# Kernel tuning notes

Measured on AMD Instinct MI355X. Metric: run time of the kernel, lower is better.

The kernel has to match this reference:

```python
import jax, jax.numpy as jnp
import numpy as np

B, N, M = 262144, 8, 4  # batch, state dim, measurement dim


def _psd(key, b, d, scale):
    # SPD matrix: A @ A^T / d + 0.1*I  (keeps inverse well-conditioned)
    A = jax.random.normal(key, (b, d, d), dtype=jnp.float32) * scale
    return A @ A.swapaxes(-1, -2) / d + 0.1 * jnp.eye(d, dtype=jnp.float32)


def setup_inputs() -> dict:
    key = jax.random.key(0)
    kF, kH, kS, kQ, kR = jax.random.split(key, 5)
    F = jax.random.normal(kF, (B, N, N), dtype=jnp.float32) * 0.3 + jnp.eye(N, dtype=jnp.float32)
    H = jax.random.normal(kH, (B, M, N), dtype=jnp.float32) * 0.5
    Sigma_previous = _psd(kS, B, N, 1.0)
    Q = _psd(kQ, B, N, 0.3)
    R = _psd(kR, B, M, 0.3)
    return {"F": F, "H": H, "Sigma_previous": Sigma_previous, "Q": Q, "R": R}


def reference(F, H, Sigma_previous, Q, R):
    T = lambda x: x.swapaxes(-1, -2)
    # predicted state covariance: Sigma = F Sigma_prev F^T + Q        [B,N,N]
    Sigma = F @ Sigma_previous @ T(F) + Q
    # innovation covariance: S = H Sigma H^T + R                      [B,M,M]
    S = H @ Sigma @ T(H) + R
    # Kalman gain: KG = Sigma H^T S^{-1}                              [B,N,M]
    P12 = Sigma @ T(H)
    KG = P12 @ jnp.linalg.inv(S)
    return KG
```

## Files before the change

kernel.cpp:

```cpp
#include <hip/hip_runtime.h>


#define NBB 16
#define THREADS 64

__device__ __forceinline__ void gl_lds16(const float* src, float4* dst) {
    __builtin_amdgcn_global_load_lds(
        (const __attribute__((address_space(1))) unsigned int*)src,
        (__attribute__((address_space(3))) unsigned int*)dst,
        16, 0, 0);
}

__global__ __launch_bounds__(THREADS) void kalman_gain_kernel(
    const float* __restrict__ Fg, const float* __restrict__ Hg,
    const float* __restrict__ Spg, const float* __restrict__ Qg,
    const float* __restrict__ Rg, float* __restrict__ out, int nb)
{
    __shared__ float4 smem4[640];

    const int lane = threadIdx.x;
    const int b0   = blockIdx.x * NBB;

    #pragma unroll
    for (int r = 0; r < 4; ++r) {
        int s = (r << 6) | lane;
        int b = s >> 4, j = s & 15, k = j ^ (b & 15);
        gl_lds16(Fg + (size_t)(b0 + b) * 64 + k * 4, smem4 + (r << 6));
    }
    #pragma unroll
    for (int r = 0; r < 2; ++r) {
        int s = (r << 6) | lane;
        int b = s >> 3, j = s & 7, k = j ^ (b & 7);
        gl_lds16(Hg + (size_t)(b0 + b) * 32 + k * 4, smem4 + 512 + (r << 6));
    }
    #pragma unroll
    for (int r = 0; r < 4; ++r) {
        int s = (r << 6) | lane;
        int b = s >> 4, j = s & 15, k = j ^ (b & 15);
        gl_lds16(Spg + (size_t)(b0 + b) * 64 + k * 4, smem4 + 256 + (r << 6));
    }

    const int b_loc = lane >> 2;
    const int p     = lane & 3;
    const int bm15  = b_loc & 15;
    const int bm7   = b_loc & 7;

    const float4 Rr = *(reinterpret_cast<const float4*>(Rg)
                        + (size_t)(b0 + b_loc) * 4 + p);

    __syncthreads();

    float hs[8];
    #pragma unroll
    for (int j = 0; j < 4; ++j) {
        float4 v = smem4[512 + b_loc * 8 + ((2 * j + (p >> 1)) ^ bm7)];
        hs[j*2+0] = (p & 1) ? v.z : v.x;
        hs[j*2+1] = (p & 1) ? v.w : v.y;
    }

    float fr[16];
    #pragma unroll
    for (int i = 0; i < 4; ++i) {
        float4 v = smem4[b_loc * 16 + ((4 * p + i) ^ bm15)];
        fr[i*4+0] = v.x; fr[i*4+1] = v.y; fr[i*4+2] = v.z; fr[i*4+3] = v.w;
    }

    float u[32];
    #pragma unroll
    for (int x = 0; x < 32; ++x) u[x] = 0.f;
    #pragma unroll
    for (int rl = 0; rl < 2; ++rl)
        #pragma unroll
        for (int k = 0; k < 8; ++k)
            #pragma unroll
            for (int j = 0; j < 4; ++j)
                u[k*4+j] += hs[j*2+rl] * fr[rl*8+k];
    #pragma unroll
    for (int x = 0; x < 32; ++x) u[x] += __shfl_xor(u[x], 1, 64);
    #pragma unroll
    for (int x = 0; x < 32; ++x) u[x] += __shfl_xor(u[x], 2, 64);

    __syncthreads();

    #pragma unroll
    for (int r = 0; r < 4; ++r) {
        int s = (r << 6) | lane;
        int b = s >> 4, j = s & 15, k = j ^ (b & 15);
        gl_lds16(Qg + (size_t)(b0 + b) * 64 + k * 4, smem4 + (r << 6));
    }

    float G[16];
    #pragma unroll
    for (int x = 0; x < 16; ++x) G[x] = 0.f;
    #pragma unroll
    for (int k = 0; k < 8; ++k) {
        float4 s0 = smem4[256 + b_loc * 16 + ((2*k    ) ^ bm15)];
        float4 s1 = smem4[256 + b_loc * 16 + ((2*k + 1) ^ bm15)];
        float sp[8] = {s0.x,s0.y,s0.z,s0.w, s1.x,s1.y,s1.z,s1.w};
        #pragma unroll
        for (int il = 0; il < 2; ++il)
            #pragma unroll
            for (int c = 0; c < 8; ++c)
                G[il*8+c] += fr[il*8+k] * sp[c];
    }

    float A[8];
    #pragma unroll
    for (int il = 0; il < 2; ++il)
        #pragma unroll
        for (int j = 0; j < 4; ++j) {
            float acc = 0.f;
            #pragma unroll
            for (int k = 0; k < 8; ++k)
                acc += G[il*8+k] * u[k*4+j];
            A[il*4+j] = acc;
        }

    __syncthreads();

    float qo[16];
    #pragma unroll
    for (int i = 0; i < 4; ++i) {
        float4 v = smem4[b_loc * 16 + ((4 * p + i) ^ bm15)];
        qo[i*4+0] = v.x; qo[i*4+1] = v.y; qo[i*4+2] = v.z; qo[i*4+3] = v.w;
    }
    #pragma unroll
    for (int j = 0; j < 4; ++j) {
        float4 h0 = smem4[512 + b_loc * 8 + ((2*j    ) ^ bm7)];
        float4 h1 = smem4[512 + b_loc * 8 + ((2*j + 1) ^ bm7)];
        float hrow[8] = {h0.x,h0.y,h0.z,h0.w, h1.x,h1.y,h1.z,h1.w};
        #pragma unroll
        for (int il = 0; il < 2; ++il) {
            float acc = 0.f;
            #pragma unroll
            for (int k = 0; k < 8; ++k)
                acc += qo[il*8+k] * hrow[k];
            A[il*4+j] += acc;
        }
    }

    float s[16];
    #pragma unroll
    for (int pi = 0; pi < 4; ++pi) {
        float rrow[4] = {Rr.x, Rr.y, Rr.z, Rr.w};
        #pragma unroll
        for (int q = 0; q < 4; ++q) {
            float acc = (pi == p) ? rrow[q] : 0.f;
            #pragma unroll
            for (int il = 0; il < 2; ++il)
                acc += hs[pi*2+il] * A[il*4+q];
            s[pi*4+q] = acc;
        }
    }
    #pragma unroll
    for (int x = 0; x < 16; ++x) s[x] += __shfl_xor(s[x], 1, 64);
    #pragma unroll
    for (int x = 0; x < 16; ++x) s[x] += __shfl_xor(s[x], 2, 64);

    float is[16] = {1.f,0.f,0.f,0.f, 0.f,1.f,0.f,0.f, 0.f,0.f,1.f,0.f, 0.f,0.f,0.f,1.f};
    #pragma unroll
    for (int c = 0; c < 4; ++c) {
        float pinv = 1.0f / s[c*4+c];
        #pragma unroll
        for (int k = 0; k < 4; ++k) { s[c*4+k] *= pinv; is[c*4+k] *= pinv; }
        #pragma unroll
        for (int r = 0; r < 4; ++r) {
            if (r != c) {
                float fac = s[r*4+c];
                #pragma unroll
                for (int k = 0; k < 4; ++k) {
                    s[r*4+k]  -= fac * s[c*4+k];
                    is[r*4+k] -= fac * is[c*4+k];
                }
            }
        }
    }

    float4* outg = reinterpret_cast<float4*>(out)
                 + (size_t)(b0 + b_loc) * 8 + 2 * p;
    #pragma unroll
    for (int il = 0; il < 2; ++il) {
        float4 o;
        o.x = A[il*4+0]*is[0] + A[il*4+1]*is[4] + A[il*4+2]*is[8]  + A[il*4+3]*is[12];
        o.y = A[il*4+0]*is[1] + A[il*4+1]*is[5] + A[il*4+2]*is[9]  + A[il*4+3]*is[13];
        o.z = A[il*4+0]*is[2] + A[il*4+1]*is[6] + A[il*4+2]*is[10] + A[il*4+3]*is[14];
        o.w = A[il*4+0]*is[3] + A[il*4+1]*is[7] + A[il*4+2]*is[11] + A[il*4+3]*is[15];
        outg[il] = o;
    }
}

extern "C" void kernel_launch(void* const* d_in, const int* in_sizes, int n_in,
                              void* d_out, int out_size, void* d_ws, size_t ws_size,
                              hipStream_t stream) {
    const float* F  = (const float*)d_in[0];
    const float* H  = (const float*)d_in[1];
    const float* Sp = (const float*)d_in[2];
    const float* Q  = (const float*)d_in[3];
    const float* R  = (const float*)d_in[4];
    float* out = (float*)d_out;

    int nb = in_sizes[0] / 64;
    int blocks = nb / NBB;
    kalman_gain_kernel<<<blocks, THREADS, 0, stream>>>(F, H, Sp, Q, R, out, nb);
}
```

Measured before the change: 52.17 us.

## Process multiple tiles per block with double-buffered async LDS prefetch

Each block now loops over 8 tiles of 16 batch elements and uses a double-buffered LDS area. The next tile's F, H, Sigma_prev and R loads are issued while the current tile computes, and manual vmcnt waits replace __syncthreads. R is now staged through LDS as well. The aim is to hide global load latency and cut block launch overhead. In exchange the grid is 8x smaller, which may reduce occupancy and parallelism, and the hand-counted waitcnt values make correctness fragile.

```diff
diff --git a/kernel.cpp b/kernel.cpp
--- a/kernel.cpp
+++ b/kernel.cpp
@@ -3,6 +3,10 @@
 
 #define NBB 16
 #define THREADS 64
+#define TILES 8
+#define BUFG 704
+
+#define WAITV(N) asm volatile("s_waitcnt vmcnt(" #N ")" ::: "memory")
 
 __device__ __forceinline__ void gl_lds16(const float* src, float4* dst) {
     __builtin_amdgcn_global_load_lds(
@@ -11,181 +15,204 @@
         16, 0, 0);
 }
 
+__device__ __forceinline__ void stage_FH(const float* Fg, const float* Hg,
+                                         float4* buf, int gb0, int lane) {
+    #pragma unroll
+    for (int r = 0; r < 4; ++r) {
+        int s = (r << 6) | lane;
+        int b = s >> 4, j = s & 15, k = j ^ (b & 15);
+        gl_lds16(Fg + (size_t)(gb0 + b) * 64 + k * 4, buf + (r << 6));
+    }
+    #pragma unroll
+    for (int r = 0; r < 2; ++r) {
+        int s = (r << 6) | lane;
+        int b = s >> 3, j = s & 7, k = j ^ (b & 7);
+        gl_lds16(Hg + (size_t)(gb0 + b) * 32 + k * 4, buf + 512 + (r << 6));
+    }
+}
+__device__ __forceinline__ void stage_SpR(const float* Spg, const float* Rg,
+                                          float4* buf, int gb0, int lane) {
+    #pragma unroll
+    for (int r = 0; r < 4; ++r) {
+        int s = (r << 6) | lane;
+        int b = s >> 4, j = s & 15, k = j ^ (b & 15);
+        gl_lds16(Spg + (size_t)(gb0 + b) * 64 + k * 4, buf + 256 + (r << 6));
+    }
+    {
+        int s = lane;
+        int b = s >> 2, j = s & 3, k = j ^ (b & 3);
+        gl_lds16(Rg + (size_t)(gb0 + b) * 16 + k * 4, buf + 640);
+    }
+}
+
 __global__ __launch_bounds__(THREADS) void kalman_gain_kernel(
     const float* __restrict__ Fg, const float* __restrict__ Hg,
     const float* __restrict__ Spg, const float* __restrict__ Qg,
     const float* __restrict__ Rg, float* __restrict__ out, int nb)
 {
-    __shared__ float4 smem4[640];
-
-    const int lane = threadIdx.x;
-    const int b0   = blockIdx.x * NBB;
-
-    #pragma unroll
-    for (int r = 0; r < 4; ++r) {
-        int s = (r << 6) | lane;
-        int b = s >> 4, j = s & 15, k = j ^ (b & 15);
-        gl_lds16(Fg + (size_t)(b0 + b) * 64 + k * 4, smem4 + (r << 6));
-    }
-    #pragma unroll
-    for (int r = 0; r < 2; ++r) {
-        int s = (r << 6) | lane;
-        int b = s >> 3, j = s & 7, k = j ^ (b & 7);
-        gl_lds16(Hg + (size_t)(b0 + b) * 32 + k * 4, smem4 + 512 + (r << 6));
-    }
-    #pragma unroll
-    for (int r = 0; r < 4; ++r) {
-        int s = (r << 6) | lane;
-        int b = s >> 4, j = s & 15, k = j ^ (b & 15);
-        gl_lds16(Spg + (size_t)(b0 + b) * 64 + k * 4, smem4 + 256 + (r << 6));
-    }
-
+    __shared__ float4 smem4[2 * BUFG];
+
+    const int lane  = threadIdx.x;
     const int b_loc = lane >> 2;
     const int p     = lane & 3;
     const int bm15  = b_loc & 15;
     const int bm7   = b_loc & 7;
-
-    const float4 Rr = *(reinterpret_cast<const float4*>(Rg)
-                        + (size_t)(b0 + b_loc) * 4 + p);
-
-    __syncthreads();
-
-    float hs[8];
-    #pragma unroll
-    for (int j = 0; j < 4; ++j) {
-        float4 v = smem4[512 + b_loc * 8 + ((2 * j + (p >> 1)) ^ bm7)];
-        hs[j*2+0] = (p & 1) ? v.z : v.x;
-        hs[j*2+1] = (p & 1) ? v.w : v.y;
-    }
-
-    float fr[16];
-    #pragma unroll
-    for (int i = 0; i < 4; ++i) {
-        float4 v = smem4[b_loc * 16 + ((4 * p + i) ^ bm15)];
-        fr[i*4+0] = v.x; fr[i*4+1] = v.y; fr[i*4+2] = v.z; fr[i*4+3] = v.w;
-    }
-
-    float u[32];
-    #pragma unroll
-    for (int x = 0; x < 32; ++x) u[x] = 0.f;
-    #pragma unroll
-    for (int rl = 0; rl < 2; ++rl)
-        #pragma unroll
-        for (int k = 0; k < 8; ++k)
-            #pragma unroll
-            for (int j = 0; j < 4; ++j)
-                u[k*4+j] += hs[j*2+rl] * fr[rl*8+k];
-    #pragma unroll
-    for (int x = 0; x < 32; ++x) u[x] += __shfl_xor(u[x], 1, 64);
-    #pragma unroll
-    for (int x = 0; x < 32; ++x) u[x] += __shfl_xor(u[x], 2, 64);
-
-    __syncthreads();
-
-    #pragma unroll
-    for (int r = 0; r < 4; ++r) {
-        int s = (r << 6) | lane;
-        int b = s >> 4, j = s & 15, k = j ^ (b & 15);
-        gl_lds16(Qg + (size_t)(b0 + b) * 64 + k * 4, smem4 + (r << 6));
-    }
-
-    float G[16];
-    #pragma unroll
-    for (int x = 0; x < 16; ++x) G[x] = 0.f;
-    #pragma unroll
-    for (int k = 0; k < 8; ++k) {
-        float4 s0 = smem4[256 + b_loc * 16 + ((2*k    ) ^ bm15)];
-        float4 s1 = smem4[256 + b_loc * 16 + ((2*k + 1) ^ bm15)];
-        float sp[8] = {s0.x,s0.y,s0.z,s0.w, s1.x,s1.y,s1.z,s1.w};
+    const int tile0 = blockIdx.x * TILES;
+
+    stage_FH (Fg,  Hg, smem4, tile0 * NBB, lane);
+    stage_SpR(Spg, Rg, smem4, tile0 * NBB, lane);
+
+    #pragma unroll 2
+    for (int t = 0; t < TILES; ++t) {
+        float4* buf  = smem4 + (t & 1) * BUFG;
+        float4* nbuf = smem4 + ((t + 1) & 1) * BUFG;
+        const int gb0 = (tile0 + t) * NBB;
+        const bool notlast = (t + 1 < TILES);
+
+        WAITV(5);
+
+        float hs[8];
+        #pragma unroll
+        for (int j = 0; j < 4; ++j) {
+            float4 v = buf[512 + b_loc * 8 + ((2 * j + (p >> 1)) ^ bm7)];
+            hs[j*2+0] = (p & 1) ? v.z : v.x;
+            hs[j*2+1] = (p & 1) ? v.w : v.y;
+        }
+        float fr[16];
+        #pragma unroll
+        for (int i = 0; i < 4; ++i) {
+            float4 v = buf[b_loc * 16 + ((4 * p + i) ^ bm15)];
+            fr[i*4+0] = v.x; fr[i*4+1] = v.y; fr[i*4+2] = v.z; fr[i*4+3] = v.w;
+        }
+        float u[32];
+        #pragma unroll
+        for (int x = 0; x < 32; ++x) u[x] = 0.f;
+        #pragma unroll
+        for (int rl = 0; rl < 2; ++rl)
+            #pragma unroll
+            for (int k = 0; k < 8; ++k)
+                #pragma unroll
+                for (int j = 0; j < 4; ++j)
+                    u[k*4+j] += hs[j*2+rl] * fr[rl*8+k];
+        #pragma unroll
+        for (int x = 0; x < 32; ++x) u[x] += __shfl_xor(u[x], 1, 64);
+        #pragma unroll
+        for (int x = 0; x < 32; ++x) u[x] += __shfl_xor(u[x], 2, 64);
+
+        asm volatile("s_waitcnt lgkmcnt(0)" ::: "memory");
+
+        #pragma unroll
+        for (int r = 0; r < 4; ++r) {
+            int s2 = (r << 6) | lane;
+            int b = s2 >> 4, j = s2 & 15, k = j ^ (b & 15);
+            gl_lds16(Qg + (size_t)(gb0 + b) * 64 + k * 4, buf + (r << 6));
+        }
+        if (notlast) {
+            stage_FH (Fg,  Hg, nbuf, gb0 + NBB, lane);
+            stage_SpR(Spg, Rg, nbuf, gb0 + NBB, lane);
+            WAITV(15);
+        } else {
+            WAITV(4);
+        }
+
+        float G[16];
+        #pragma unroll
+        for (int x = 0; x < 16; ++x) G[x] = 0.f;
+        #pragma unroll
+        for (int k = 0; k < 8; ++k) {
+            float4 s0 = buf[256 + b_loc * 16 + ((2*k    ) ^ bm15)];
+            float4 s1 = buf[256 + b_loc * 16 + ((2*k + 1) ^ bm15)];
+            float sp[8] = {s0.x,s0.y,s0.z,s0.w, s1.x,s1.y,s1.z,s1.w};
+            #pragma unroll
+            for (int il = 0; il < 2; ++il)
+                #pragma unroll
+                for (int c = 0; c < 8; ++c)
+                    G[il*8+c] += fr[il*8+k] * sp[c];
+        }
+        float A[8];
         #pragma unroll
         for (int il = 0; il < 2; ++il)
             #pragma unroll
-            for (int c = 0; c < 8; ++c)
-                G[il*8+c] += fr[il*8+k] * sp[c];
-    }
-
-    float A[8];
-    #pragma unroll
-    for (int il = 0; il < 2; ++il)
+            for (int j = 0; j < 4; ++j) {
+                float acc = 0.f;
+                #pragma unroll
+                for (int k = 0; k < 8; ++k)
+                    acc += G[il*8+k] * u[k*4+j];
+                A[il*4+j] = acc;
+            }
+
+        if (notlast) { WAITV(11); } else { WAITV(0); }
+
+        float qo[16];
+        #pragma unroll
+        for (int i = 0; i < 4; ++i) {
+            float4 v = buf[b_loc * 16 + ((4 * p + i) ^ bm15)];
+            qo[i*4+0] = v.x; qo[i*4+1] = v.y; qo[i*4+2] = v.z; qo[i*4+3] = v.w;
+        }
         #pragma unroll
         for (int j = 0; j < 4; ++j) {
-            float acc = 0.f;
-            #pragma unroll
-            for (int k = 0; k < 8; ++k)
-                acc += G[il*8+k] * u[k*4+j];
-            A[il*4+j] = acc;
-        }
-
-    __syncthreads();
-
-    float qo[16];
-    #pragma unroll
-    for (int i = 0; i < 4; ++i) {
-        float4 v = smem4[b_loc * 16 + ((4 * p + i) ^ bm15)];
-        qo[i*4+0] = v.x; qo[i*4+1] = v.y; qo[i*4+2] = v.z; qo[i*4+3] = v.w;
-    }
-    #pragma unroll
-    for (int j = 0; j < 4; ++j) {
-        float4 h0 = smem4[512 + b_loc * 8 + ((2*j    ) ^ bm7)];
-        float4 h1 = smem4[512 + b_loc * 8 + ((2*j + 1) ^ bm7)];
-        float hrow[8] = {h0.x,h0.y,h0.z,h0.w, h1.x,h1.y,h1.z,h1.w};
+            float4 h0 = buf[512 + b_loc * 8 + ((2*j    ) ^ bm7)];
+            float4 h1 = buf[512 + b_loc * 8 + ((2*j + 1) ^ bm7)];
+            float hrow[8] = {h0.x,h0.y,h0.z,h0.w, h1.x,h1.y,h1.z,h1.w};
+            #pragma unroll
+            for (int il = 0; il < 2; ++il) {
+                float acc = 0.f;
+                #pragma unroll
+                for (int k = 0; k < 8; ++k)
+                    acc += qo[il*8+k] * hrow[k];
+                A[il*4+j] += acc;
+            }
+        }
+        float4 Rr = buf[640 + b_loc * 4 + (p ^ (b_loc & 3))];
+        float s[16];
+        #pragma unroll
+        for (int pi = 0; pi < 4; ++pi) {
+            float rrow[4] = {Rr.x, Rr.y, Rr.z, Rr.w};
+            #pragma unroll
+            for (int q = 0; q < 4; ++q) {
+                float acc = (pi == p) ? rrow[q] : 0.f;
+                #pragma unroll
+                for (int il = 0; il < 2; ++il)
+                    acc += hs[pi*2+il] * A[il*4+q];
+                s[pi*4+q] = acc;
+            }
+        }
+        #pragma unroll
+        for (int x = 0; x < 16; ++x) s[x] += __shfl_xor(s[x], 1, 64);
+        #pragma unroll
+        for (int x = 0; x < 16; ++x) s[x] += __shfl_xor(s[x], 2, 64);
+
+        float is[16] = {1.f,0.f,0.f,0.f, 0.f,1.f,0.f,0.f,
+                        0.f,0.f,1.f,0.f, 0.f,0.f,0.f,1.f};
+        #pragma unroll
+        for (int c = 0; c < 4; ++c) {
+            float pinv = 1.0f / s[c*4+c];
+            #pragma unroll
+            for (int k = 0; k < 4; ++k) { s[c*4+k] *= pinv; is[c*4+k] *= pinv; }
+            #pragma unroll
+            for (int r = 0; r < 4; ++r) {
+                if (r != c) {
+                    float fac = s[r*4+c];
+                    #pragma unroll
+                    for (int k = 0; k < 4; ++k) {
+                        s[r*4+k]  -= fac * s[c*4+k];
+                        is[r*4+k] -= fac * is[c*4+k];
+                    }
+                }
+            }
+        }
+
+        float4* outg = reinterpret_cast<float4*>(out)
+                     + (size_t)(gb0 + b_loc) * 8 + 2 * p;
         #pragma unroll
         for (int il = 0; il < 2; ++il) {
-            float acc = 0.f;
-            #pragma unroll
-            for (int k = 0; k < 8; ++k)
-                acc += qo[il*8+k] * hrow[k];
-            A[il*4+j] += acc;
-        }
-    }
-
-    float s[16];
-    #pragma unroll
-    for (int pi = 0; pi < 4; ++pi) {
-        float rrow[4] = {Rr.x, Rr.y, Rr.z, Rr.w};
-        #pragma unroll
-        for (int q = 0; q < 4; ++q) {
-            float acc = (pi == p) ? rrow[q] : 0.f;
-            #pragma unroll
-            for (int il = 0; il < 2; ++il)
-                acc += hs[pi*2+il] * A[il*4+q];
-            s[pi*4+q] = acc;
-        }
-    }
-    #pragma unroll
-    for (int x = 0; x < 16; ++x) s[x] += __shfl_xor(s[x], 1, 64);
-    #pragma unroll
-    for (int x = 0; x < 16; ++x) s[x] += __shfl_xor(s[x], 2, 64);
-
-    float is[16] = {1.f,0.f,0.f,0.f, 0.f,1.f,0.f,0.f, 0.f,0.f,1.f,0.f, 0.f,0.f,0.f,1.f};
-    #pragma unroll
-    for (int c = 0; c < 4; ++c) {
-        float pinv = 1.0f / s[c*4+c];
-        #pragma unroll
-        for (int k = 0; k < 4; ++k) { s[c*4+k] *= pinv; is[c*4+k] *= pinv; }
-        #pragma unroll
-        for (int r = 0; r < 4; ++r) {
-            if (r != c) {
-                float fac = s[r*4+c];
-                #pragma unroll
-                for (int k = 0; k < 4; ++k) {
-                    s[r*4+k]  -= fac * s[c*4+k];
-                    is[r*4+k] -= fac * is[c*4+k];
-                }
-            }
-        }
-    }
-
-    float4* outg = reinterpret_cast<float4*>(out)
-                 + (size_t)(b0 + b_loc) * 8 + 2 * p;
-    #pragma unroll
-    for (int il = 0; il < 2; ++il) {
-        float4 o;
-        o.x = A[il*4+0]*is[0] + A[il*4+1]*is[4] + A[il*4+2]*is[8]  + A[il*4+3]*is[12];
-        o.y = A[il*4+0]*is[1] + A[il*4+1]*is[5] + A[il*4+2]*is[9]  + A[il*4+3]*is[13];
-        o.z = A[il*4+0]*is[2] + A[il*4+1]*is[6] + A[il*4+2]*is[10] + A[il*4+3]*is[14];
-        o.w = A[il*4+0]*is[3] + A[il*4+1]*is[7] + A[il*4+2]*is[11] + A[il*4+3]*is[15];
-        outg[il] = o;
+            float4 o;
+            o.x = A[il*4+0]*is[0] + A[il*4+1]*is[4] + A[il*4+2]*is[8]  + A[il*4+3]*is[12];
+            o.y = A[il*4+0]*is[1] + A[il*4+1]*is[5] + A[il*4+2]*is[9]  + A[il*4+3]*is[13];
+            o.z = A[il*4+0]*is[2] + A[il*4+1]*is[6] + A[il*4+2]*is[10] + A[il*4+3]*is[14];
+            o.w = A[il*4+0]*is[3] + A[il*4+1]*is[7] + A[il*4+2]*is[11] + A[il*4+3]*is[15];
+            outg[il] = o;
+        }
     }
 }
 
@@ -200,6 +227,6 @@
     float* out = (float*)d_out;
 
     int nb = in_sizes[0] / 64;
-    int blocks = nb / NBB;
+    int blocks = nb / (NBB * TILES);
     kalman_gain_kernel<<<blocks, THREADS, 0, stream>>>(F, H, Sp, Q, R, out, nb);
 }
```

Measured after the change: 67.73 us. 1.3x slower.
